# Optimization experiments

Hardware: AMD Instinct MI355X
Metric: run time of the kernel (lower is better)

## Reference

```python
import jax, jax.numpy as jnp
import numpy as np

B, S, D, H = 4, 2048, 1024, 16
DK = D // H

def setup_inputs() -> dict:
    key = jax.random.key(0)
    ks = jax.random.split(key, 5)
    scale = 0.02
    return {
        "x": jax.random.normal(ks[0], (B, S, D), dtype=jnp.float32),
        "Wqkv": jax.random.normal(ks[1], (3 * D, D), dtype=jnp.float32) * scale,
        "bqkv": jax.random.normal(ks[2], (3 * D,), dtype=jnp.float32) * scale,
        "Wout": jax.random.normal(ks[3], (D, D), dtype=jnp.float32) * scale,
        "bout": jax.random.normal(ks[4], (D,), dtype=jnp.float32) * scale,
    }

def reference(x, Wqkv, bqkv, Wout, bout):
    # fused QKV projection: [B,S,3D]
    qkv = jnp.einsum('bsd,ed->bse', x, Wqkv) + bqkv
    q, k, v = jnp.split(qkv, 3, axis=-1)
    # [B,S,D] -> [B,H,S,DK]
    def heads(t):
        return t.reshape(B, S, H, DK).transpose(0, 2, 1, 3)
    q, k, v = heads(q), heads(k), heads(v)
    # scaled dot-product attention (no mask, no dropout)
    scores = jnp.einsum('bhqd,bhkd->bhqk', q, k) / jnp.sqrt(jnp.float32(DK))
    attn = jax.nn.softmax(scores, axis=-1)
    out = jnp.einsum('bhqk,bhkd->bhqd', attn, v)
    # merge heads -> [B,S,D]
    out = out.transpose(0, 2, 1, 3).reshape(B, S, D)
    return jnp.einsum('bsd,ed->bse', out, Wout) + bout
```

## Files before the change

kernel.cpp:

```cpp
#include <hip/hip_runtime.h>
#include <hip/hip_bf16.h>
#include <cstdint>
#include <cstddef>

typedef __bf16 bf16_t;
typedef bf16_t bf16x8 __attribute__((ext_vector_type(8)));
typedef bf16_t bf16x4 __attribute__((ext_vector_type(4)));
typedef bf16_t bf16x2 __attribute__((ext_vector_type(2)));
typedef float f32x4 __attribute__((ext_vector_type(4)));
typedef float f32x16 __attribute__((ext_vector_type(16)));
typedef unsigned int u32x4 __attribute__((ext_vector_type(4)));

#define B_  4
#define S_  2048
#define D_  1024
#define H_  16
#define DK_ 64

#define QSCALE 0.18033688011112042f

__device__ __forceinline__ void gload_lds16(const bf16_t* g, bf16_t* l) {
  __builtin_amdgcn_global_load_lds(
      (__attribute__((address_space(1))) void*)(void*)g,
      (__attribute__((address_space(3))) void*)(void*)l,
      16, 0, 0);
}

__device__ __forceinline__ f32x4 mfma_bf16(bf16x8 a, bf16x8 b, f32x4 c) {
  return __builtin_amdgcn_mfma_f32_16x16x32_bf16(a, b, c, 0, 0, 0);
}
__device__ __forceinline__ f32x16 mfma32(bf16x8 a, bf16x8 b, f32x16 c) {
  return __builtin_amdgcn_mfma_f32_32x32x16_bf16(a, b, c, 0, 0, 0);
}

__device__ __forceinline__ unsigned pk2(float a, float b) {
  bf16x2 v; v[0] = (bf16_t)a; v[1] = (bf16_t)b;
  return __builtin_bit_cast(unsigned, v);
}

__device__ __forceinline__ void pl32(unsigned &a, unsigned &b) {
  auto r = __builtin_amdgcn_permlane32_swap((int)a, (int)b, false, false);
  a = (unsigned)r[0];
  b = (unsigned)r[1];
}

#define NQ_X  2097152
#define NQ_WQ  786432
#define NQ_WO  262144
__global__ void cvt_all(const float* __restrict__ x, const float* __restrict__ wq,
                        const float* __restrict__ wo,
                        bf16_t* __restrict__ xb, bf16_t* __restrict__ wqb,
                        bf16_t* __restrict__ wob) {
  int i = blockIdx.x * blockDim.x + threadIdx.x;
  const float* src;
  bf16_t* dst;
  if (i < NQ_X)                  { src = x;  dst = xb; }
  else if (i < NQ_X + NQ_WQ)     { src = wq; dst = wqb; i -= NQ_X; }
  else if (i < NQ_X + NQ_WQ + NQ_WO) { src = wo; dst = wob; i -= (NQ_X + NQ_WQ); }
  else return;
  float4 v = reinterpret_cast<const float4*>(src)[i];
  bf16x4 o;
  o[0] = (bf16_t)v.x; o[1] = (bf16_t)v.y; o[2] = (bf16_t)v.z; o[3] = (bf16_t)v.w;
  reinterpret_cast<bf16x4*>(dst)[i] = o;
}


__global__ __launch_bounds__(256) void gemm_qkv(
    const bf16_t* __restrict__ A, const bf16_t* __restrict__ Bm,
    const float* __restrict__ bias,
    bf16_t* __restrict__ Qf, bf16_t* __restrict__ Kf, bf16_t* __restrict__ Vf) {
  __shared__ bf16_t As[128 * 32];
  __shared__ bf16_t Bs[128 * 32];
  const int t = threadIdx.x;
  const int l = t & 63;
  const int w = t >> 6;
  const int wm = w >> 1, wn = w & 1;
  const int fr = l & 15, fh = l >> 4;
  const int bid = (int)blockIdx.x;
  const int swz = (bid & 7) * 192 + (bid >> 3);
  const int m0 = (swz / 24) * 128, n0 = (swz % 24) * 128;
  const int K = 1024;
  const int ar = t >> 2, ak = (t & 3) * 8;

  f32x4 acc[4][4] = {};

  for (int k0 = 0; k0 < K; k0 += 32) {
    gload_lds16(A + (size_t)(m0 + ar) * K + k0 + ak,        &As[t * 8]);
    gload_lds16(A + (size_t)(m0 + 64 + ar) * K + k0 + ak,   &As[2048 + t * 8]);
    gload_lds16(Bm + (size_t)(n0 + ar) * K + k0 + ak,       &Bs[t * 8]);
    gload_lds16(Bm + (size_t)(n0 + 64 + ar) * K + k0 + ak,  &Bs[2048 + t * 8]);
    __syncthreads();
    bf16x8 af[4], bfv[4];
#pragma unroll
    for (int i = 0; i < 4; ++i)
      af[i] = *reinterpret_cast<const bf16x8*>(&As[(wm * 64 + i * 16 + fr) * 32 + fh * 8]);
#pragma unroll
    for (int i = 0; i < 4; ++i)
      bfv[i] = *reinterpret_cast<const bf16x8*>(&Bs[(wn * 64 + i * 16 + fr) * 32 + fh * 8]);
#pragma unroll
    for (int mi = 0; mi < 4; ++mi)
#pragma unroll
      for (int ni = 0; ni < 4; ++ni)
        acc[mi][ni] = mfma_bf16(af[mi], bfv[ni], acc[mi][ni]);
    __syncthreads();
  }

#pragma unroll
  for (int mi = 0; mi < 4; ++mi) {
#pragma unroll
    for (int ni = 0; ni < 4; ++ni) {
      const int e = n0 + wn * 64 + ni * 16 + fr;
      const int sec = e >> 10;
      const int h = (e & 1023) >> 6, dk = e & 63;
      const float bv = bias[e];
#pragma unroll
      for (int j = 0; j < 4; ++j) {
        const int m = m0 + wm * 64 + mi * 16 + fh * 4 + j;
        const int b = m >> 11, s = m & 2047;
        const float val = acc[mi][ni][j] + bv;
        const size_t hb = (size_t)(b * H_ + h) * (S_ * DK_);
        if (sec == 2) {
          const int tv = s >> 5, tt = (s >> 4) & 1, jj = dk >> 5;
          const int lane = (dk & 31) + ((s >> 3) & 1) * 32, el = s & 7;
          Vf[hb + (size_t)((((tv * 2 + tt) * 2 + jj) * 64 + lane) * 8 + el)] = (bf16_t)val;
        } else {
          const int tq = s >> 5, d = dk >> 4;
          const int lane = (s & 31) + ((dk >> 3) & 1) * 32, el = dk & 7;
          const size_t idx = hb + (size_t)(((tq * 4 + d) * 64 + lane) * 8 + el);
          if (sec == 0) Qf[idx] = (bf16_t)(val * QSCALE);
          else          Kf[idx] = (bf16_t)val;
        }
      }
    }
  }
}

__global__ __launch_bounds__(256) void gemm_out(
    const bf16_t* __restrict__ A, const bf16_t* __restrict__ Bm,
    const float* __restrict__ bias, float* __restrict__ out) {
  __shared__ bf16_t As[128 * 32];
  __shared__ bf16_t Bs[128 * 32];
  const int t = threadIdx.x;
  const int l = t & 63;
  const int w = t >> 6;
  const int wm = w >> 1, wn = w & 1;
  const int fr = l & 15, fh = l >> 4;
  const int bid = (int)blockIdx.x;
  const int swz = (bid & 7) * 64 + (bid >> 3);
  const int m0 = (swz >> 3) * 128, n0 = (swz & 7) * 128;
  const int K = 1024;
  const int ar = t >> 2, ak = (t & 3) * 8;

  f32x4 acc[4][4] = {};

  for (int k0 = 0; k0 < K; k0 += 32) {
    gload_lds16(A + (size_t)(m0 + ar) * K + k0 + ak,        &As[t * 8]);
    gload_lds16(A + (size_t)(m0 + 64 + ar) * K + k0 + ak,   &As[2048 + t * 8]);
    gload_lds16(Bm + (size_t)(n0 + ar) * K + k0 + ak,       &Bs[t * 8]);
    gload_lds16(Bm + (size_t)(n0 + 64 + ar) * K + k0 + ak,  &Bs[2048 + t * 8]);
    __syncthreads();
    bf16x8 af[4], bfv[4];
#pragma unroll
    for (int i = 0; i < 4; ++i)
      af[i] = *reinterpret_cast<const bf16x8*>(&As[(wm * 64 + i * 16 + fr) * 32 + fh * 8]);
#pragma unroll
    for (int i = 0; i < 4; ++i)
      bfv[i] = *reinterpret_cast<const bf16x8*>(&Bs[(wn * 64 + i * 16 + fr) * 32 + fh * 8]);
#pragma unroll
    for (int mi = 0; mi < 4; ++mi)
#pragma unroll
      for (int ni = 0; ni < 4; ++ni)
        acc[mi][ni] = mfma_bf16(af[mi], bfv[ni], acc[mi][ni]);
    __syncthreads();
  }

#pragma unroll
  for (int mi = 0; mi < 4; ++mi) {
#pragma unroll
    for (int ni = 0; ni < 4; ++ni) {
      const int e = n0 + wn * 64 + ni * 16 + fr;
      const float bv = bias[e];
#pragma unroll
      for (int j = 0; j < 4; ++j) {
        const int m = m0 + wm * 64 + mi * 16 + fh * 4 + j;
        out[(size_t)m * D_ + e] = acc[mi][ni][j] + bv;
      }
    }
  }
}

__global__ __launch_bounds__(256, 4) void attn_fwd(
    const bf16_t* __restrict__ Qf, const bf16_t* __restrict__ Kf,
    const bf16_t* __restrict__ Vf, bf16_t* __restrict__ Aout) {
  const int t = threadIdx.x, l = t & 63, w = t >> 6;
  const int lq = l & 31, hi = l >> 5;
  const int bid = (int)blockIdx.x;
  const int swz = (bid & 7) * 128 + (bid >> 3);
  const int bh = swz >> 4;
  const int q0 = (swz & 15) * 128 + w * 32;
  const int b = bh >> 4, h = bh & 15;

  const bf16_t* Qh = Qf + (size_t)bh * (S_ * DK_);
  const bf16_t* Kh = Kf + (size_t)bh * (S_ * DK_) + (size_t)l * 8;
  const bf16_t* Vh = Vf + (size_t)bh * (S_ * DK_) + (size_t)l * 8;

  const int tq = q0 >> 5;
  bf16x8 qf[4];
#pragma unroll
  for (int d = 0; d < 4; ++d)
    qf[d] = *reinterpret_cast<const bf16x8*>(&Qh[(size_t)(((tq * 4 + d) * 64 + l) * 8)]);

  f32x16 oa0 = {}, oa1 = {};
  float m = -1e30f, rs = 0.f;

  bf16x8 kA0, kA1, kA2, kA3, kB0, kB1, kB2, kB3;
  kA0 = *reinterpret_cast<const bf16x8*>(&Kh[0 * 512]);
  kA1 = *reinterpret_cast<const bf16x8*>(&Kh[1 * 512]);
  kA2 = *reinterpret_cast<const bf16x8*>(&Kh[2 * 512]);
  kA3 = *reinterpret_cast<const bf16x8*>(&Kh[3 * 512]);

#define ATTN_PHASE(KC0, KC1, KC2, KC3, KN0, KN1, KN2, KN3, CUR, NXT)                      \
  {                                                                                        \
    KN0 = *reinterpret_cast<const bf16x8*>(&Kh[(size_t)(((NXT) * 4 + 0) * 512)]);          \
    KN1 = *reinterpret_cast<const bf16x8*>(&Kh[(size_t)(((NXT) * 4 + 1) * 512)]);          \
    KN2 = *reinterpret_cast<const bf16x8*>(&Kh[(size_t)(((NXT) * 4 + 2) * 512)]);          \
    KN3 = *reinterpret_cast<const bf16x8*>(&Kh[(size_t)(((NXT) * 4 + 3) * 512)]);          \
    bf16x8 v00 = *reinterpret_cast<const bf16x8*>(&Vh[(size_t)((((CUR) * 2 + 0) * 2 + 0) * 512)]); \
    bf16x8 v01 = *reinterpret_cast<const bf16x8*>(&Vh[(size_t)((((CUR) * 2 + 0) * 2 + 1) * 512)]); \
    bf16x8 v10 = *reinterpret_cast<const bf16x8*>(&Vh[(size_t)((((CUR) * 2 + 1) * 2 + 0) * 512)]); \
    bf16x8 v11 = *reinterpret_cast<const bf16x8*>(&Vh[(size_t)((((CUR) * 2 + 1) * 2 + 1) * 512)]); \
    __builtin_amdgcn_s_setprio(1);                                                         \
    f32x16 cs = {};                                                                        \
    cs = mfma32(KC0, qf[0], cs);                                                           \
    cs = mfma32(KC1, qf[1], cs);                                                           \
    cs = mfma32(KC2, qf[2], cs);                                                           \
    cs = mfma32(KC3, qf[3], cs);                                                           \
    __builtin_amdgcn_s_setprio(0);                                                         \
    float t0 = fmaxf(fmaxf(cs[0], cs[1]), cs[2]);                                          \
    float t1 = fmaxf(fmaxf(cs[3], cs[4]), cs[5]);                                          \
    float t2 = fmaxf(fmaxf(cs[6], cs[7]), cs[8]);                                          \
    float t3 = fmaxf(fmaxf(cs[9], cs[10]), cs[11]);                                        \
    float t4 = fmaxf(fmaxf(cs[12], cs[13]), cs[14]);                                       \
    float tm = fmaxf(fmaxf(fmaxf(t0, t1), cs[15]), fmaxf(fmaxf(t2, t3), t4));              \
    if (__any(tm > m + 8.f)) {                                                             \
      _Pragma("unroll")                                                                    \
      for (int sh = 1; sh < 64; sh <<= 1) tm = fmaxf(tm, __shfl_xor(tm, sh));              \
      const float alpha = __builtin_amdgcn_exp2f(m - tm);                                  \
      m = tm; rs *= alpha;                                                                 \
      _Pragma("unroll")                                                                    \
      for (int r = 0; r < 16; ++r) { oa0[r] *= alpha; oa1[r] *= alpha; }                   \
    }                                                                                      \
    float pv[16];                                                                          \
    _Pragma("unroll")                                                                      \
    for (int r = 0; r < 16; ++r) pv[r] = __builtin_amdgcn_exp2f(cs[r] - m);                \
    {                                                                                      \
      float s0 = pv[0] + pv[1],   s1 = pv[2] + pv[3];                                      \
      float s2 = pv[4] + pv[5],   s3 = pv[6] + pv[7];                                      \
      float s4 = pv[8] + pv[9],   s5 = pv[10] + pv[11];                                    \
      float s6 = pv[12] + pv[13], s7 = pv[14] + pv[15];                                    \
      rs += ((s0 + s1) + (s2 + s3)) + ((s4 + s5) + (s6 + s7));                             \
    }                                                                                      \
    _Pragma("unroll")                                                                      \
    for (int tt = 0; tt < 2; ++tt) {                                                       \
      unsigned A0 = pk2(pv[8 * tt],     pv[8 * tt + 1]);                                   \
      unsigned B0 = pk2(pv[8 * tt + 2], pv[8 * tt + 3]);                                   \
      unsigned A1 = pk2(pv[8 * tt + 4], pv[8 * tt + 5]);                                   \
      unsigned B1 = pk2(pv[8 * tt + 6], pv[8 * tt + 7]);                                   \
      pl32(A0, A1);                                                                        \
      pl32(B0, B1);                                                                        \
      u32x4 fw;                                                                            \
      fw[0] = A0; fw[1] = B0; fw[2] = A1; fw[3] = B1;                                      \
      const bf16x8 pa = __builtin_bit_cast(bf16x8, fw);                                    \
      __builtin_amdgcn_s_setprio(1);                                                       \
      oa0 = mfma32(pa, (tt ? v10 : v00), oa0);                                             \
      oa1 = mfma32(pa, (tt ? v11 : v01), oa1);                                             \
      __builtin_amdgcn_s_setprio(0);                                                       \
    }                                                                                      \
  }

  for (int it = 0; it < 64; it += 2) {
    ATTN_PHASE(kA0, kA1, kA2, kA3, kB0, kB1, kB2, kB3, it, it + 1)
    ATTN_PHASE(kB0, kB1, kB2, kB3, kA0, kA1, kA2, kA3, it + 1, (it + 2) & 63)
  }
#undef ATTN_PHASE

  rs += __shfl_xor(rs, 32);
  const float inv = 1.0f / rs;
#pragma unroll
  for (int r = 0; r < 16; ++r) {
    const int ql = (r & 3) + 8 * (r >> 2) + 4 * hi;
    const float ir = __shfl(inv, ql);
    const size_t row = (size_t)(b * S_ + q0 + ql) * D_ + h * 64 + lq;
    Aout[row]      = (bf16_t)(oa0[r] * ir);
    Aout[row + 32] = (bf16_t)(oa1[r] * ir);
  }
}

extern "C" void kernel_launch(void* const* d_in, const int* in_sizes, int n_in,
                              void* d_out, int out_size, void* d_ws, size_t ws_size,
                              hipStream_t stream) {
  const float* x    = (const float*)d_in[0];
  const float* Wqkv = (const float*)d_in[1];
  const float* bqkv = (const float*)d_in[2];
  const float* Wout = (const float*)d_in[3];
  const float* bout = (const float*)d_in[4];
  float* out = (float*)d_out;

  char* ws = (char*)d_ws;
  bf16_t* xb    = (bf16_t*)(ws);
  bf16_t* wqkvb = (bf16_t*)(ws + 16777216);
  bf16_t* woutb = (bf16_t*)(ws + 23068672);
  bf16_t* Qfr   = (bf16_t*)(ws + 25165824);
  bf16_t* Kfr   = (bf16_t*)(ws + 41943040);
  bf16_t* Vfr   = (bf16_t*)(ws + 58720256);
  bf16_t* aout  = (bf16_t*)(ws + 75497472);

  cvt_all<<<12288, 256, 0, stream>>>(x, Wqkv, Wout, xb, wqkvb, woutb);

  gemm_qkv<<<1536, 256, 0, stream>>>(xb, wqkvb, bqkv, Qfr, Kfr, Vfr);
  attn_fwd<<<1024, 256, 0, stream>>>(Qfr, Kfr, Vfr, aout);
  gemm_out<<<512, 256, 0, stream>>>(aout, woutb, bout, out);
}
```

Before: 200.7 us.

## Restructure projection GEMMs with double-buffered LDS, 128x256 tiles and phased MFMA scheduling

```diff
diff --git a/kernel.cpp b/kernel.cpp
--- a/kernel.cpp
+++ b/kernel.cpp
@@ -65,45 +65,102 @@
 }
 
 
-__global__ __launch_bounds__(256) void gemm_qkv(
+#define GSTAGE_A(KT, BUF, I, APTR)                                                         \
+  gload_lds16((APTR) + (size_t)(m0 + (I) * 64 + (t >> 3)) * 1024 + (KT) * 64 + xg,        \
+              &As[BUF][(I) * 4096 + t * 8]);
+#define GSTAGE_B(KT, BUF, J, BPTR)                                                         \
+  gload_lds16((BPTR) + (size_t)(n0 + (J) * 64 + (t >> 3)) * 1024 + (KT) * 64 + xg,        \
+              &Bs[BUF][(J) * 4096 + t * 8]);
+
+#define PH_BAR                                                                             \
+  asm volatile("" ::: "memory");                                                           \
+  __builtin_amdgcn_s_barrier();                                                            \
+  asm volatile("" ::: "memory");
+
+#define PH_MFMA(MI, A0, A1)                                                                \
+  __builtin_amdgcn_s_setprio(1);                                                           \
+  _Pragma("unroll")                                                                        \
+  for (int ni = 0; ni < 4; ++ni) {                                                         \
+    acc[MI][ni] = mfma_bf16(A0, bfr[ni][0], acc[MI][ni]);                                  \
+    acc[MI][ni] = mfma_bf16(A1, bfr[ni][1], acc[MI][ni]);                                  \
+  }                                                                                        \
+  __builtin_amdgcn_s_setprio(0);
+
+#define GEMM_BODY(APTR, BPTR)                                                              \
+  GSTAGE_A(0, 0, 0, APTR) GSTAGE_A(0, 0, 1, APTR)                                          \
+  GSTAGE_B(0, 0, 0, BPTR) GSTAGE_B(0, 0, 1, BPTR)                                          \
+  GSTAGE_B(0, 0, 2, BPTR) GSTAGE_B(0, 0, 3, BPTR)                                          \
+  for (int kt = 0; kt < 16; ++kt) {                                                        \
+    const int cur = kt & 1, nb = cur ^ 1, nkt = (kt + 1) & 15;                             \
+    const bf16_t* Ac = &As[cur][0];                                                        \
+    const bf16_t* Bc = &Bs[cur][0];                                                        \
+                \
+    GSTAGE_A(nkt, nb, 0, APTR) GSTAGE_A(nkt, nb, 1, APTR)                                  \
+    asm volatile("s_waitcnt vmcnt(2)" ::: "memory");                                       \
+    PH_BAR                                                                                 \
+    bf16x8 bfr[4][2];                                                                      \
+    _Pragma("unroll")                                                                      \
+    for (int ni = 0; ni < 4; ++ni) {                                                       \
+      bfr[ni][0] = *reinterpret_cast<const bf16x8*>(&Bc[rbB + ni * 1024 + c0]);            \
+      bfr[ni][1] = *reinterpret_cast<const bf16x8*>(&Bc[rbB + ni * 1024 + c1]);            \
+    }                                                                                      \
+    {                                                                                      \
+      bf16x8 a0 = *reinterpret_cast<const bf16x8*>(&Ac[raB + 0 * 1024 + c0]);              \
+      bf16x8 a1 = *reinterpret_cast<const bf16x8*>(&Ac[raB + 0 * 1024 + c1]);              \
+      PH_MFMA(0, a0, a1)                                                                   \
+    }                                                                                      \
+    PH_BAR                                                                                 \
+                                                 \
+    {                                                                                      \
+      bf16x8 a0 = *reinterpret_cast<const bf16x8*>(&Ac[raB + 1 * 1024 + c0]);              \
+      bf16x8 a1 = *reinterpret_cast<const bf16x8*>(&Ac[raB + 1 * 1024 + c1]);              \
+      GSTAGE_B(nkt, nb, 0, BPTR) GSTAGE_B(nkt, nb, 1, BPTR)                                \
+      PH_BAR                                                                               \
+      PH_MFMA(1, a0, a1)                                                                   \
+      PH_BAR                                                                               \
+    }                                                                                      \
+                                                 \
+    {                                                                                      \
+      bf16x8 a0 = *reinterpret_cast<const bf16x8*>(&Ac[raB + 2 * 1024 + c0]);              \
+      bf16x8 a1 = *reinterpret_cast<const bf16x8*>(&Ac[raB + 2 * 1024 + c1]);              \
+      GSTAGE_B(nkt, nb, 2, BPTR) GSTAGE_B(nkt, nb, 3, BPTR)                                \
+      PH_BAR                                                                               \
+      PH_MFMA(2, a0, a1)                                                                   \
+      PH_BAR                                                                               \
+    }                                                                                      \
+                                                              \
+    {                                                                                      \
+      bf16x8 a0 = *reinterpret_cast<const bf16x8*>(&Ac[raB + 3 * 1024 + c0]);              \
+      bf16x8 a1 = *reinterpret_cast<const bf16x8*>(&Ac[raB + 3 * 1024 + c1]);              \
+      PH_BAR                                                                               \
+      PH_MFMA(3, a0, a1)                                                                   \
+      PH_BAR                                                                               \
+    }                                                                                      \
+  }
+
+__global__ __launch_bounds__(512, 2) void gemm_qkv(
     const bf16_t* __restrict__ A, const bf16_t* __restrict__ Bm,
     const float* __restrict__ bias,
     bf16_t* __restrict__ Qf, bf16_t* __restrict__ Kf, bf16_t* __restrict__ Vf) {
-  __shared__ bf16_t As[128 * 32];
-  __shared__ bf16_t Bs[128 * 32];
+  __shared__ bf16_t As[2][128 * 64];
+  __shared__ bf16_t Bs[2][256 * 64];
   const int t = threadIdx.x;
   const int l = t & 63;
   const int w = t >> 6;
-  const int wm = w >> 1, wn = w & 1;
+  const int wm = w >> 2, wn = w & 3;
   const int fr = l & 15, fh = l >> 4;
   const int bid = (int)blockIdx.x;
-  const int swz = (bid & 7) * 192 + (bid >> 3);
-  const int m0 = (swz / 24) * 128, n0 = (swz % 24) * 128;
-  const int K = 1024;
-  const int ar = t >> 2, ak = (t & 3) * 8;
+  const int swz = (bid & 7) * 96 + (bid >> 3);
+  const int m0 = (swz / 12) * 128, n0 = (swz % 12) * 256;
+  const int xg = (((t & 7) ^ ((t >> 3) & 7)) * 8);
+  const int c0 = ((fh) ^ (fr & 7)) * 8;
+  const int c1 = ((4 + fh) ^ (fr & 7)) * 8;
+  const int raB = (wm * 64 + fr) * 64;
+  const int rbB = (wn * 64 + fr) * 64;
 
   f32x4 acc[4][4] = {};
 
-  for (int k0 = 0; k0 < K; k0 += 32) {
-    gload_lds16(A + (size_t)(m0 + ar) * K + k0 + ak,        &As[t * 8]);
-    gload_lds16(A + (size_t)(m0 + 64 + ar) * K + k0 + ak,   &As[2048 + t * 8]);
-    gload_lds16(Bm + (size_t)(n0 + ar) * K + k0 + ak,       &Bs[t * 8]);
-    gload_lds16(Bm + (size_t)(n0 + 64 + ar) * K + k0 + ak,  &Bs[2048 + t * 8]);
-    __syncthreads();
-    bf16x8 af[4], bfv[4];
-#pragma unroll
-    for (int i = 0; i < 4; ++i)
-      af[i] = *reinterpret_cast<const bf16x8*>(&As[(wm * 64 + i * 16 + fr) * 32 + fh * 8]);
-#pragma unroll
-    for (int i = 0; i < 4; ++i)
-      bfv[i] = *reinterpret_cast<const bf16x8*>(&Bs[(wn * 64 + i * 16 + fr) * 32 + fh * 8]);
-#pragma unroll
-    for (int mi = 0; mi < 4; ++mi)
-#pragma unroll
-      for (int ni = 0; ni < 4; ++ni)
-        acc[mi][ni] = mfma_bf16(af[mi], bfv[ni], acc[mi][ni]);
-    __syncthreads();
-  }
+  GEMM_BODY(A, Bm)
 
 #pragma unroll
   for (int mi = 0; mi < 4; ++mi) {
@@ -135,44 +192,28 @@
   }
 }
 
-__global__ __launch_bounds__(256) void gemm_out(
+__global__ __launch_bounds__(512, 2) void gemm_out(
     const bf16_t* __restrict__ A, const bf16_t* __restrict__ Bm,
     const float* __restrict__ bias, float* __restrict__ out) {
-  __shared__ bf16_t As[128 * 32];
-  __shared__ bf16_t Bs[128 * 32];
+  __shared__ bf16_t As[2][128 * 64];
+  __shared__ bf16_t Bs[2][256 * 64];
   const int t = threadIdx.x;
   const int l = t & 63;
   const int w = t >> 6;
-  const int wm = w >> 1, wn = w & 1;
+  const int wm = w >> 2, wn = w & 3;
   const int fr = l & 15, fh = l >> 4;
   const int bid = (int)blockIdx.x;
-  const int swz = (bid & 7) * 64 + (bid >> 3);
-  const int m0 = (swz >> 3) * 128, n0 = (swz & 7) * 128;
-  const int K = 1024;
-  const int ar = t >> 2, ak = (t & 3) * 8;
+  const int swz = (bid & 7) * 32 + (bid >> 3);
+  const int m0 = (swz >> 2) * 128, n0 = (swz & 3) * 256;
+  const int xg = (((t & 7) ^ ((t >> 3) & 7)) * 8);
+  const int c0 = ((fh) ^ (fr & 7)) * 8;
+  const int c1 = ((4 + fh) ^ (fr & 7)) * 8;
+  const int raB = (wm * 64 + fr) * 64;
+  const int rbB = (wn * 64 + fr) * 64;
 
   f32x4 acc[4][4] = {};
 
-  for (int k0 = 0; k0 < K; k0 += 32) {
-    gload_lds16(A + (size_t)(m0 + ar) * K + k0 + ak,        &As[t * 8]);
-    gload_lds16(A + (size_t)(m0 + 64 + ar) * K + k0 + ak,   &As[2048 + t * 8]);
-    gload_lds16(Bm + (size_t)(n0 + ar) * K + k0 + ak,       &Bs[t * 8]);
-    gload_lds16(Bm + (size_t)(n0 + 64 + ar) * K + k0 + ak,  &Bs[2048 + t * 8]);
-    __syncthreads();
-    bf16x8 af[4], bfv[4];
-#pragma unroll
-    for (int i = 0; i < 4; ++i)
-      af[i] = *reinterpret_cast<const bf16x8*>(&As[(wm * 64 + i * 16 + fr) * 32 + fh * 8]);
-#pragma unroll
-    for (int i = 0; i < 4; ++i)
-      bfv[i] = *reinterpret_cast<const bf16x8*>(&Bs[(wn * 64 + i * 16 + fr) * 32 + fh * 8]);
-#pragma unroll
-    for (int mi = 0; mi < 4; ++mi)
-#pragma unroll
-      for (int ni = 0; ni < 4; ++ni)
-        acc[mi][ni] = mfma_bf16(af[mi], bfv[ni], acc[mi][ni]);
-    __syncthreads();
-  }
+  GEMM_BODY(A, Bm)
 
 #pragma unroll
   for (int mi = 0; mi < 4; ++mi) {
@@ -317,7 +358,7 @@
 
   cvt_all<<<12288, 256, 0, stream>>>(x, Wqkv, Wout, xb, wqkvb, woutb);
 
-  gemm_qkv<<<1536, 256, 0, stream>>>(xb, wqkvb, bqkv, Qfr, Kfr, Vfr);
+  gemm_qkv<<<768, 512, 0, stream>>>(xb, wqkvb, bqkv, Qfr, Kfr, Vfr);
   attn_fwd<<<1024, 256, 0, stream>>>(Qfr, Kfr, Vfr, aout);
-  gemm_out<<<512, 256, 0, stream>>>(aout, woutb, bout, out);
-}
+  gemm_out<<<256, 512, 0, stream>>>(aout, woutb, bout, out);
+}
```

After: 207.6 us. 1.03x slower.
